# Optimization experiments

Hardware: AMD Instinct MI355X
Metric: run time of the kernel (lower is better)

## Reference

```python
import jax, jax.numpy as jnp
import numpy as np

# norse LIFParameters defaults with v_th overridden to 0.23
DT = 1e-3
TAU_SYN_INV = 200.0   # 1/5e-3
TAU_MEM_INV = 100.0   # 1/1e-2
V_TH = 0.23
ENC_V_TH = 1.0        # encoder uses default LIFParameters (v_th=1.0)
SEQ_LEN = 24
HIDDEN = 256
N_CLASSES = 10


def heaviside(x):
    return (x > 0).astype(x.dtype)


def encode(x):
    """ConstantCurrentLIFEncoder: lif_current_encoder over SEQ_LEN steps. x: [B, F] -> [T, B, F] spikes."""
    def step(v, _):
        v = v + DT * TAU_MEM_INV * (x - v)          # dv = dt*tau_mem_inv*((v_leak - v) + I)
        z = heaviside(v - ENC_V_TH)
        v = (1.0 - z) * v                            # reset to v_reset = 0
        return v, z
    _, zs = jax.lax.scan(step, jnp.zeros_like(x), None, length=SEQ_LEN)
    return zs


def lif_ff_step(inp, v, i):
    """norse lif_feed_forward_step: decay v with old i, decay i, spike, reset, then add input to i."""
    v_dec = v + DT * TAU_MEM_INV * (i - v)           # v_leak = 0
    i_dec = i * (1.0 - DT * TAU_SYN_INV)
    z = heaviside(v_dec - V_TH)
    v_new = (1.0 - z) * v_dec                        # v_reset = 0
    i_new = i_dec + inp
    return z, v_new, i_new


def setup_inputs() -> dict:
    key = jax.random.key(0)
    ks = jax.random.split(key, 8)
    B, F = 4096, 1024
    def lin(k, fan_in, fan_out):
        bound = 1.0 / np.sqrt(fan_in)
        kw, kb = jax.random.split(k)
        W = jax.random.uniform(kw, (fan_out, fan_in), jnp.float32, -bound, bound)
        b = jax.random.uniform(kb, (fan_out,), jnp.float32, -bound, bound)
        return W, b
    x = jax.random.normal(ks[0], (B, F), jnp.float32)
    W1, b1 = lin(ks[1], F, HIDDEN)
    W2, b2 = lin(ks[2], HIDDEN, HIDDEN)
    W3, b3 = lin(ks[3], HIDDEN, HIDDEN)
    Wli = jax.random.normal(ks[4], (N_CLASSES, HIDDEN), jnp.float32) * np.sqrt(2.0 / HIDDEN)
    return {"x": x, "W1": W1, "b1": b1, "W2": W2, "b2": b2, "W3": W3, "b3": b3, "Wli": Wli}


def reference(x, W1, b1, W2, b2, W3, b3, Wli):
    # dropout layers are identity in eval mode
    enc = encode(x)                                   # [T, B, F]
    B = x.shape[0]
    z2 = lambda d: jnp.zeros((B, d), x.dtype)
    carry0 = (z2(HIDDEN), z2(HIDDEN), z2(HIDDEN), z2(HIDDEN), z2(HIDDEN), z2(HIDDEN),
              z2(N_CLASSES), z2(N_CLASSES))
    def step(c, z):
        v1, i1, v2, i2, v3, i3, vo, io = c
        o1, v1, i1 = lif_ff_step(z @ W1.T + b1, v1, i1)
        o2, v2, i2 = lif_ff_step(o1 @ W2.T + b2, v2, i2)
        o2 = o2 + o1                                  # residual
        o3, v3, i3 = lif_ff_step(o2 @ W3.T + b3, v3, i3)
        o3 = o3 + o2                                  # residual
        # LILinearCell li_step: v from old i, i decays then accumulates W @ input (no bias)
        vo = vo + DT * TAU_MEM_INV * (io - vo)
        io = io * (1.0 - DT * TAU_SYN_INV) + o3 @ Wli.T
        return (v1, i1, v2, i2, v3, i3, vo, io), vo
    _, voltages = jax.lax.scan(step, carry0, enc)     # [T, B, n_classes]
    return voltages[-1]                               # decode = last timestep
```

## Files before the change

kernel.cpp:

```cpp
#include <hip/hip_runtime.h>
#include <hip/hip_bf16.h>

#define FEAT   1024
#define HID    256
#define TSTEPS 24
#define NCLS   10

typedef unsigned int u32;
typedef unsigned long long u64;
typedef unsigned short u16;

constexpr int OFF_W1T  = 0;
constexpr int OFF_W2T  = OFF_W1T + FEAT*HID;
constexpr int OFF_W3T  = OFF_W2T + HID*HID;
constexpr int OFF_WLI  = OFF_W3T + HID*HID;
constexpr int OFF_B1   = OFF_WLI + NCLS*HID;
constexpr int OFF_B2   = OFF_B1 + HID;
constexpr int OFF_B3   = OFF_B2 + HID;

struct CoefT { float c[TSTEPS]; };
constexpr CoefT make_coef() {
    CoefT r{};
    double c = 0.0, p9 = 1.0;
    r.c[TSTEPS-1] = 0.0f;
    for (int u = TSTEPS-1; u > 0; u--) {
        c = 0.8 * c + 0.1 * p9;
        p9 *= 0.9;
        r.c[u-1] = (float)c;
    }
    return r;
}
__device__ constexpr CoefT COEF = make_coef();

__device__ __forceinline__ u32 detect_bf16(const void* __restrict__ x, u32 lane) {
    float v = __bfloat162float(((const __hip_bfloat16*)x)[lane]);
    u64 bad = __ballot(!(fabsf(v) < 100.0f));
    return bad == 0ull ? 1u : 0u;
}

__device__ __forceinline__ float rd_any(const void* p, int idx, u32 isbf) {
    return isbf ? __bfloat162float(((const __hip_bfloat16*)p)[idx])
                : ((const float*)p)[idx];
}

__global__ __launch_bounds__(256) void prep_weights_k(const void* __restrict__ x,
        const void* W1, const void* W2, const void* W3, const void* Wli,
        const void* b1, const void* b2, const void* b3, float* __restrict__ ws) {
    const u32 isbf = detect_bf16(x, threadIdx.x & 63);
    const int b = blockIdx.x;
    const u32 tid = threadIdx.x;

    if (b == 96) {
        for (u32 e = tid; e < NCLS*HID; e += 256) ws[OFF_WLI + e] = rd_any(Wli, e, isbf);
        for (u32 e = tid; e < 3*HID; e += 256) {
            u32 which = e >> 8, idx = e & 255;
            const void* src = which == 0 ? b1 : (which == 1 ? b2 : b3);
            int off = which == 0 ? OFF_B1 : (which == 1 ? OFF_B2 : OFF_B3);
            ws[off + idx] = rd_any(src, idx, isbf);
        }
        return;
    }

    const void* src; float* dst; int srcW, h0, f0;
    if (b < 64)      { src = W1; dst = ws + OFF_W1T; srcW = FEAT; h0 = (b >> 4) * 64; f0 = (b & 15) * 64; }
    else if (b < 80) { int tb = b - 64; src = W2; dst = ws + OFF_W2T; srcW = HID; h0 = (tb >> 2) * 64; f0 = (tb & 3) * 64; }
    else             { int tb = b - 80; src = W3; dst = ws + OFF_W3T; srcW = HID; h0 = (tb >> 2) * 64; f0 = (tb & 3) * 64; }

    __shared__ float sm[64][65];
    const u32 c = tid & 63, r0 = tid >> 6;
    #pragma unroll
    for (int i = 0; i < 16; i++) {
        u32 r = r0 + 4 * i;
        sm[r][c] = rd_any(src, (h0 + r) * srcW + f0 + c, isbf);
    }
    __syncthreads();
    #pragma unroll
    for (int i = 0; i < 16; i++) {
        u32 r = r0 + 4 * i;
        dst[(size_t)(f0 + r) * HID + h0 + c] = sm[c][r];
    }
}

template<int SH, int MJ>
__device__ __forceinline__ void gather_stream(float acc[4], const float* __restrict__ Wt,
                                              u32 lm, u32 lane4) {
    u64 act = __ballot(lm != 0u);
    if (!act) return;
    u32 p = (u32)__builtin_ctzll(act); act &= act - 1;
    u32 cur = (u32)__builtin_amdgcn_readlane((int)lm, (int)p);
    for (;;) {
        u32 j = (u32)__builtin_ctz(cur); cur &= cur - 1;
        const u32 c0 = (p << SH) + (j & (u32)MJ);
        u32 c1 = c0, c2 = c0, c3 = c0;
        float f1 = 0.f, f2 = 0.f, f3 = 0.f;
        if (cur || act) {
            if (!cur) { p = (u32)__builtin_ctzll(act); act &= act - 1;
                        cur = (u32)__builtin_amdgcn_readlane((int)lm, (int)p); }
            j = (u32)__builtin_ctz(cur); cur &= cur - 1;
            c1 = (p << SH) + (j & (u32)MJ); f1 = 1.f;
        }
        if (cur || act) {
            if (!cur) { p = (u32)__builtin_ctzll(act); act &= act - 1;
                        cur = (u32)__builtin_amdgcn_readlane((int)lm, (int)p); }
            j = (u32)__builtin_ctz(cur); cur &= cur - 1;
            c2 = (p << SH) + (j & (u32)MJ); f2 = 1.f;
        }
        if (cur || act) {
            if (!cur) { p = (u32)__builtin_ctzll(act); act &= act - 1;
                        cur = (u32)__builtin_amdgcn_readlane((int)lm, (int)p); }
            j = (u32)__builtin_ctz(cur); cur &= cur - 1;
            c3 = (p << SH) + (j & (u32)MJ); f3 = 1.f;
        }
        const float4 w0 = *(const float4*)(Wt + ((size_t)c0 << 8) + lane4);
        const float4 w1 = *(const float4*)(Wt + ((size_t)c1 << 8) + lane4);
        const float4 w2 = *(const float4*)(Wt + ((size_t)c2 << 8) + lane4);
        const float4 w3 = *(const float4*)(Wt + ((size_t)c3 << 8) + lane4);
        acc[0] += w0.x; acc[1] += w0.y; acc[2] += w0.z; acc[3] += w0.w;
        acc[0] = fmaf(f1, w1.x, acc[0]); acc[1] = fmaf(f1, w1.y, acc[1]);
        acc[2] = fmaf(f1, w1.z, acc[2]); acc[3] = fmaf(f1, w1.w, acc[3]);
        acc[0] = fmaf(f2, w2.x, acc[0]); acc[1] = fmaf(f2, w2.y, acc[1]);
        acc[2] = fmaf(f2, w2.z, acc[2]); acc[3] = fmaf(f2, w2.w, acc[3]);
        acc[0] = fmaf(f3, w3.x, acc[0]); acc[1] = fmaf(f3, w3.y, acc[1]);
        acc[2] = fmaf(f3, w3.z, acc[2]); acc[3] = fmaf(f3, w3.w, acc[3]);
        if (!cur && !act) return;
        if (!cur) { p = (u32)__builtin_ctzll(act); act &= act - 1;
                    cur = (u32)__builtin_amdgcn_readlane((int)lm, (int)p); }
    }
}

__global__ __launch_bounds__(256) void snn_k(const void* __restrict__ xin,
                                             const float* __restrict__ ws,
                                             void* __restrict__ out) {
    const u32 tid  = threadIdx.x;
    const u32 lane = tid & 63;
    const u32 wv   = tid >> 6;
    const int row  = blockIdx.x * 4 + wv;
    const u32 lane4 = lane * 4;
    const u32 isbf = detect_bf16(xin, lane);

    const float* __restrict__ W1T = ws + OFF_W1T;
    const float* __restrict__ W2T = ws + OFF_W2T;
    const float* __restrict__ W3T = ws + OFF_W3T;
    const float* __restrict__ WLI = ws + OFF_WLI;

    __shared__ u32 sched[12 * 256];

    {
        float xv[16];
        if (isbf) {
            const uint4* xp = (const uint4*)((const u16*)xin + (size_t)row*FEAT + lane*16);
            uint4 A = xp[0], B = xp[1];
            u32 w[8] = {A.x, A.y, A.z, A.w, B.x, B.y, B.z, B.w};
            #pragma unroll
            for (int i = 0; i < 8; i++) {
                xv[2*i]   = __uint_as_float(w[i] << 16);
                xv[2*i+1] = __uint_as_float(w[i] & 0xffff0000u);
            }
        } else {
            const float4* xp = (const float4*)((const float*)xin + (size_t)row*FEAT + lane*16);
            float4 A = xp[0], B = xp[1], C = xp[2], D = xp[3];
            float tmp[16] = {A.x,A.y,A.z,A.w,B.x,B.y,B.z,B.w,C.x,C.y,C.z,C.w,D.x,D.y,D.z,D.w};
            #pragma unroll
            for (int i = 0; i < 16; i++) xv[i] = tmp[i];
        }
        u32 smreg[12];
        #pragma unroll
        for (int i = 0; i < 12; i++) smreg[i] = 0;
        #pragma unroll
        for (int j = 0; j < 16; j++) {
            float v = 0.f;
            #pragma unroll
            for (int t = 0; t < TSTEPS; t++) {
                v = v + 0.1f * (xv[j] - v);
                bool z = v > 1.0f;
                v = z ? 0.0f : v;
                if (z) smreg[t >> 1] |= 1u << (((t & 1) << 4) + j);
            }
        }
        #pragma unroll
        for (int i = 0; i < 12; i++) sched[i * 256 + tid] = smreg[i];
    }

    float v1[4], i1[4], v2[4], i2[4], v3[4], i3[4], g[4];
    #pragma unroll
    for (int k = 0; k < 4; k++) {
        v1[k]=0.f; i1[k]=0.f; v2[k]=0.f; i2[k]=0.f; v3[k]=0.f; i3[k]=0.f; g[k]=0.f;
    }
    const float4 b1v = *(const float4*)(ws + OFF_B1 + lane4);
    const float4 b2v = *(const float4*)(ws + OFF_B2 + lane4);
    const float4 b3v = *(const float4*)(ws + OFF_B3 + lane4);

    u32 pairreg = 0;
    for (int t = 0; t < TSTEPS; t++) {
        if ((t & 1) == 0) pairreg = sched[(t >> 1) * 256 + tid];
        const u32 lmE = (t & 1) ? (pairreg >> 16) : (pairreg & 0xffffu);

        float a1[4] = {b1v.x, b1v.y, b1v.z, b1v.w};
        gather_stream<4, 15>(a1, W1T, lmE, lane4);

        float o1v[4]; u32 lm1 = 0;
        #pragma unroll
        for (int kk = 0; kk < 4; kk++) {
            float vd = v1[kk] + 0.1f * (i1[kk] - v1[kk]);
            i1[kk] = i1[kk] * 0.8f;
            bool z = vd > 0.23f;
            v1[kk] = z ? 0.0f : vd;
            i1[kk] = i1[kk] + a1[kk];
            o1v[kk] = z ? 1.0f : 0.0f;
            lm1 |= (z ? 1u : 0u) << kk;
        }

        float a2[4] = {b2v.x, b2v.y, b2v.z, b2v.w};
        gather_stream<2, 3>(a2, W2T, lm1, lane4);

        float o2v[4]; u32 lm2 = 0;
        #pragma unroll
        for (int kk = 0; kk < 4; kk++) {
            float vd = v2[kk] + 0.1f * (i2[kk] - v2[kk]);
            i2[kk] = i2[kk] * 0.8f;
            bool z = vd > 0.23f;
            v2[kk] = z ? 0.0f : vd;
            i2[kk] = i2[kk] + a2[kk];
            o2v[kk] = (z ? 1.0f : 0.0f) + o1v[kk];
            lm2 |= (z ? 1u : 0u) << kk;
        }

        float a3[4] = {b3v.x, b3v.y, b3v.z, b3v.w};
        gather_stream<2, 3>(a3, W3T, lm2 | (lm1 << 4), lane4);

        const float cf = COEF.c[t];
        #pragma unroll
        for (int kk = 0; kk < 4; kk++) {
            float vd = v3[kk] + 0.1f * (i3[kk] - v3[kk]);
            i3[kk] = i3[kk] * 0.8f;
            bool z = vd > 0.23f;
            v3[kk] = z ? 0.0f : vd;
            i3[kk] = i3[kk] + a3[kk];
            float o3 = (z ? 1.0f : 0.0f) + o2v[kk];
            g[kk] += cf * o3;
        }
    }

    float s[NCLS];
    #pragma unroll
    for (int c = 0; c < NCLS; c++) {
        const float4 w = *(const float4*)(WLI + c*HID + lane4);
        float p = g[0]*w.x + g[1]*w.y + g[2]*w.z + g[3]*w.w;
        #pragma unroll
        for (int d = 32; d > 0; d >>= 1) p += __shfl_xor(p, d, 64);
        s[c] = p;
    }
    if (lane == 0) {
        if (isbf) {
            __hip_bfloat16* o = (__hip_bfloat16*)out + (size_t)row*NCLS;
            #pragma unroll
            for (int c = 0; c < NCLS; c++) o[c] = __float2bfloat16(s[c]);
        } else {
            float* o = (float*)out + (size_t)row*NCLS;
            #pragma unroll
            for (int c = 0; c < NCLS; c++) o[c] = s[c];
        }
    }
}

extern "C" void kernel_launch(void* const* d_in, const int* in_sizes, int n_in,
                              void* d_out, int out_size, void* d_ws, size_t ws_size,
                              hipStream_t stream) {
    const void* x   = d_in[0];
    const void* W1  = d_in[1];
    const void* b1  = d_in[2];
    const void* W2  = d_in[3];
    const void* b2  = d_in[4];
    const void* W3  = d_in[5];
    const void* b3  = d_in[6];
    const void* Wli = d_in[7];
    float* ws = (float*)d_ws;
    const int batch = in_sizes[0] / FEAT;

    prep_weights_k<<<97, 256, 0, stream>>>(x, W1, W2, W3, Wli, b1, b2, b3, ws);
    snn_k<<<batch/4, 256, 0, stream>>>(x, ws, d_out);
}
```

Before: 177.8 us.

## Build compacted spike index lists in LDS and gather weights in chunks of eight

Replaces the serial ballot/readlane spike iteration with a per-wave prefix-sum (mbcnt over popcount bits) that writes compacted active-column indices into shared memory, then gathers weight rows eight at a time with packed float2 accumulation. Layer 3 merges duplicate columns from the residual (o1+o2) into one entry with a multiplicity weight instead of two loads. The prep kernel also switches from an LDS-tiled transpose to a simple scattered-write transpose with more blocks. It adds LDS traffic and extra ballots per step but aims to remove scalar loop overhead and raise memory-level parallelism in the gathers.

```diff
diff --git a/kernel.cpp b/kernel.cpp
--- a/kernel.cpp
+++ b/kernel.cpp
@@ -9,6 +9,7 @@
 typedef unsigned int u32;
 typedef unsigned long long u64;
 typedef unsigned short u16;
+typedef float v2f __attribute__((ext_vector_type(2)));
 
 constexpr int OFF_W1T  = 0;
 constexpr int OFF_W2T  = OFF_W1T + FEAT*HID;
@@ -43,88 +44,129 @@
                 : ((const float*)p)[idx];
 }
 
-__global__ __launch_bounds__(256) void prep_weights_k(const void* __restrict__ x,
+__device__ __forceinline__ float4 rd4(const void* p, int i, u32 isbf) {
+    if (isbf) {
+        const u32* q = (const u32*)p;
+        u32 a = q[i >> 1], b = q[(i >> 1) + 1];
+        float4 r;
+        r.x = __uint_as_float(a << 16); r.y = __uint_as_float(a & 0xffff0000u);
+        r.z = __uint_as_float(b << 16); r.w = __uint_as_float(b & 0xffff0000u);
+        return r;
+    }
+    return ((const float4*)p)[i >> 2];
+}
+
+__global__ __launch_bounds__(256) void prep_k(const void* __restrict__ x,
         const void* W1, const void* W2, const void* W3, const void* Wli,
         const void* b1, const void* b2, const void* b3, float* __restrict__ ws) {
     const u32 isbf = detect_bf16(x, threadIdx.x & 63);
-    const int b = blockIdx.x;
-    const u32 tid = threadIdx.x;
-
-    if (b == 96) {
-        for (u32 e = tid; e < NCLS*HID; e += 256) ws[OFF_WLI + e] = rd_any(Wli, e, isbf);
-        for (u32 e = tid; e < 3*HID; e += 256) {
-            u32 which = e >> 8, idx = e & 255;
-            const void* src = which == 0 ? b1 : (which == 1 ? b2 : b3);
-            int off = which == 0 ? OFF_B1 : (which == 1 ? OFF_B2 : OFF_B3);
-            ws[off + idx] = rd_any(src, idx, isbf);
-        }
+    int b = blockIdx.x;
+    const u32 t = threadIdx.x;
+    if (b < 256) {
+        int id = b * 256 + t;
+        int h = id >> 8, f4 = (id & 255) << 2;
+        float4 w = rd4(W1, h * FEAT + f4, isbf);
+        float* d = ws + OFF_W1T;
+        d[(f4+0)*HID + h] = w.x; d[(f4+1)*HID + h] = w.y;
+        d[(f4+2)*HID + h] = w.z; d[(f4+3)*HID + h] = w.w;
         return;
     }
-
-    const void* src; float* dst; int srcW, h0, f0;
-    if (b < 64)      { src = W1; dst = ws + OFF_W1T; srcW = FEAT; h0 = (b >> 4) * 64; f0 = (b & 15) * 64; }
-    else if (b < 80) { int tb = b - 64; src = W2; dst = ws + OFF_W2T; srcW = HID; h0 = (tb >> 2) * 64; f0 = (tb & 3) * 64; }
-    else             { int tb = b - 80; src = W3; dst = ws + OFF_W3T; srcW = HID; h0 = (tb >> 2) * 64; f0 = (tb & 3) * 64; }
-
-    __shared__ float sm[64][65];
-    const u32 c = tid & 63, r0 = tid >> 6;
+    b -= 256;
+    if (b < 64) {
+        int id = b * 256 + t;
+        int h = id >> 6, f4 = (id & 63) << 2;
+        float4 w = rd4(W2, h * HID + f4, isbf);
+        float* d = ws + OFF_W2T;
+        d[(f4+0)*HID + h] = w.x; d[(f4+1)*HID + h] = w.y;
+        d[(f4+2)*HID + h] = w.z; d[(f4+3)*HID + h] = w.w;
+        return;
+    }
+    b -= 64;
+    if (b < 64) {
+        int id = b * 256 + t;
+        int h = id >> 6, f4 = (id & 63) << 2;
+        float4 w = rd4(W3, h * HID + f4, isbf);
+        float* d = ws + OFF_W3T;
+        d[(f4+0)*HID + h] = w.x; d[(f4+1)*HID + h] = w.y;
+        d[(f4+2)*HID + h] = w.z; d[(f4+3)*HID + h] = w.w;
+        return;
+    }
+    for (u32 e = t; e < NCLS*HID; e += 256) ws[OFF_WLI + e] = rd_any(Wli, e, isbf);
+    ws[OFF_B1 + t] = rd_any(b1, t, isbf);
+    ws[OFF_B2 + t] = rd_any(b2, t, isbf);
+    ws[OFF_B3 + t] = rd_any(b3, t, isbf);
+}
+
+__device__ __forceinline__ u32 mbcnt64(u64 m) {
+    return __builtin_amdgcn_mbcnt_hi((u32)(m >> 32),
+           __builtin_amdgcn_mbcnt_lo((u32)m, 0u));
+}
+
+
+__device__ __forceinline__ u32 build_list4(u16* list, u32 lmA, u32 lmB, u32 lane) {
+    u32 u = lmA | lmB;
+    u32 cnt = (u32)__builtin_popcount(u);
+    u64 B0 = __ballot((cnt & 1u) != 0);
+    u64 B1 = __ballot((cnt & 2u) != 0);
+    u64 B2 = __ballot((cnt & 4u) != 0);
+    u32 pos = mbcnt64(B0) + 2u*mbcnt64(B1) + 4u*mbcnt64(B2);
+    u32 n = (u32)__builtin_popcountll(B0) + 2u*(u32)__builtin_popcountll(B1)
+          + 4u*(u32)__builtin_popcountll(B2);
+    while (u) {
+        u32 j = (u32)__builtin_ctz(u); u &= u - 1;
+        u32 mult = ((lmA >> j) & 1u) + ((lmB >> j) & 1u);
+        list[pos++] = (u16)(((lane << 2) + j) | (mult << 12));
+    }
+    u32 pad = (8u - (n & 7u)) & 7u;
+    if (lane < pad) list[n + lane] = 0;
+    return n;
+}
+
+__device__ __forceinline__ u32 build_listE(u16* list, u32 lm, u32 lane) {
+    u32 cnt = (u32)__builtin_popcount(lm);
+    u32 pos = 0, n = 0;
     #pragma unroll
-    for (int i = 0; i < 16; i++) {
-        u32 r = r0 + 4 * i;
-        sm[r][c] = rd_any(src, (h0 + r) * srcW + f0 + c, isbf);
-    }
-    __syncthreads();
-    #pragma unroll
-    for (int i = 0; i < 16; i++) {
-        u32 r = r0 + 4 * i;
-        dst[(size_t)(f0 + r) * HID + h0 + c] = sm[c][r];
-    }
-}
-
-template<int SH, int MJ>
-__device__ __forceinline__ void gather_stream(float acc[4], const float* __restrict__ Wt,
-                                              u32 lm, u32 lane4) {
-    u64 act = __ballot(lm != 0u);
-    if (!act) return;
-    u32 p = (u32)__builtin_ctzll(act); act &= act - 1;
-    u32 cur = (u32)__builtin_amdgcn_readlane((int)lm, (int)p);
-    for (;;) {
-        u32 j = (u32)__builtin_ctz(cur); cur &= cur - 1;
-        const u32 c0 = (p << SH) + (j & (u32)MJ);
-        u32 c1 = c0, c2 = c0, c3 = c0;
-        float f1 = 0.f, f2 = 0.f, f3 = 0.f;
-        if (cur || act) {
-            if (!cur) { p = (u32)__builtin_ctzll(act); act &= act - 1;
-                        cur = (u32)__builtin_amdgcn_readlane((int)lm, (int)p); }
-            j = (u32)__builtin_ctz(cur); cur &= cur - 1;
-            c1 = (p << SH) + (j & (u32)MJ); f1 = 1.f;
-        }
-        if (cur || act) {
-            if (!cur) { p = (u32)__builtin_ctzll(act); act &= act - 1;
-                        cur = (u32)__builtin_amdgcn_readlane((int)lm, (int)p); }
-            j = (u32)__builtin_ctz(cur); cur &= cur - 1;
-            c2 = (p << SH) + (j & (u32)MJ); f2 = 1.f;
-        }
-        if (cur || act) {
-            if (!cur) { p = (u32)__builtin_ctzll(act); act &= act - 1;
-                        cur = (u32)__builtin_amdgcn_readlane((int)lm, (int)p); }
-            j = (u32)__builtin_ctz(cur); cur &= cur - 1;
-            c3 = (p << SH) + (j & (u32)MJ); f3 = 1.f;
-        }
-        const float4 w0 = *(const float4*)(Wt + ((size_t)c0 << 8) + lane4);
-        const float4 w1 = *(const float4*)(Wt + ((size_t)c1 << 8) + lane4);
-        const float4 w2 = *(const float4*)(Wt + ((size_t)c2 << 8) + lane4);
-        const float4 w3 = *(const float4*)(Wt + ((size_t)c3 << 8) + lane4);
-        acc[0] += w0.x; acc[1] += w0.y; acc[2] += w0.z; acc[3] += w0.w;
-        acc[0] = fmaf(f1, w1.x, acc[0]); acc[1] = fmaf(f1, w1.y, acc[1]);
-        acc[2] = fmaf(f1, w1.z, acc[2]); acc[3] = fmaf(f1, w1.w, acc[3]);
-        acc[0] = fmaf(f2, w2.x, acc[0]); acc[1] = fmaf(f2, w2.y, acc[1]);
-        acc[2] = fmaf(f2, w2.z, acc[2]); acc[3] = fmaf(f2, w2.w, acc[3]);
-        acc[0] = fmaf(f3, w3.x, acc[0]); acc[1] = fmaf(f3, w3.y, acc[1]);
-        acc[2] = fmaf(f3, w3.z, acc[2]); acc[3] = fmaf(f3, w3.w, acc[3]);
-        if (!cur && !act) return;
-        if (!cur) { p = (u32)__builtin_ctzll(act); act &= act - 1;
-                    cur = (u32)__builtin_amdgcn_readlane((int)lm, (int)p); }
+    for (int b = 0; b < 5; b++) {
+        u64 B = __ballot(((cnt >> b) & 1u) != 0);
+        pos += mbcnt64(B) << b;
+        n += ((u32)__builtin_popcountll(B)) << b;
+    }
+    while (lm) {
+        u32 j = (u32)__builtin_ctz(lm); lm &= lm - 1;
+        list[pos++] = (u16)(((lane << 4) + j) | 0x1000u);
+    }
+    u32 pad = (8u - (n & 7u)) & 7u;
+    if (lane < pad) list[n + lane] = 0;
+    return n;
+}
+
+#define GSTEP(E, W) do { \
+    float mm = (float)((E) >> 12); \
+    v2f mv = {mm, mm}; \
+    v2f lo = {(W).x, (W).y}, hi = {(W).z, (W).w}; \
+    accA += mv * lo; accB += mv * hi; \
+} while (0)
+
+__device__ __forceinline__ void gather_list(v2f& accA, v2f& accB,
+        const float* __restrict__ Wt, const u16* list, u32 n, u32 lane4) {
+    u32 nch = (n + 7u) >> 3;
+    const uint4* lp = (const uint4*)list;
+    for (u32 c = 0; c < nch; c++) {
+        uint4 d = lp[c];
+        u32 e0 = d.x & 0xffffu, e1 = d.x >> 16;
+        u32 e2 = d.y & 0xffffu, e3 = d.y >> 16;
+        u32 e4 = d.z & 0xffffu, e5 = d.z >> 16;
+        u32 e6 = d.w & 0xffffu, e7 = d.w >> 16;
+        const float4 w0 = *(const float4*)(Wt + ((e0 & 0xfffu) << 8) + lane4);
+        const float4 w1 = *(const float4*)(Wt + ((e1 & 0xfffu) << 8) + lane4);
+        const float4 w2 = *(const float4*)(Wt + ((e2 & 0xfffu) << 8) + lane4);
+        const float4 w3 = *(const float4*)(Wt + ((e3 & 0xfffu) << 8) + lane4);
+        const float4 w4 = *(const float4*)(Wt + ((e4 & 0xfffu) << 8) + lane4);
+        const float4 w5 = *(const float4*)(Wt + ((e5 & 0xfffu) << 8) + lane4);
+        const float4 w6 = *(const float4*)(Wt + ((e6 & 0xfffu) << 8) + lane4);
+        const float4 w7 = *(const float4*)(Wt + ((e7 & 0xfffu) << 8) + lane4);
+        GSTEP(e0, w0); GSTEP(e1, w1); GSTEP(e2, w2); GSTEP(e3, w3);
+        GSTEP(e4, w4); GSTEP(e5, w5); GSTEP(e6, w6); GSTEP(e7, w7);
     }
 }
 
@@ -144,6 +186,8 @@
     const float* __restrict__ WLI = ws + OFF_WLI;
 
     __shared__ u32 sched[12 * 256];
+    __shared__ __align__(16) u16 listE[4][1040];
+    __shared__ __align__(16) u16 listL[4][272];
 
     {
         float xv[16];
@@ -190,13 +234,18 @@
     const float4 b2v = *(const float4*)(ws + OFF_B2 + lane4);
     const float4 b3v = *(const float4*)(ws + OFF_B3 + lane4);
 
+    u16* const lE = listE[wv];
+    u16* const lL = listL[wv];
+
     u32 pairreg = 0;
     for (int t = 0; t < TSTEPS; t++) {
         if ((t & 1) == 0) pairreg = sched[(t >> 1) * 256 + tid];
         const u32 lmE = (t & 1) ? (pairreg >> 16) : (pairreg & 0xffffu);
 
-        float a1[4] = {b1v.x, b1v.y, b1v.z, b1v.w};
-        gather_stream<4, 15>(a1, W1T, lmE, lane4);
+        u32 nE = build_listE(lE, lmE, lane);
+        v2f accA = {b1v.x, b1v.y}, accB = {b1v.z, b1v.w};
+        gather_list(accA, accB, W1T, lE, nE, lane4);
+        float a1[4] = {accA.x, accA.y, accB.x, accB.y};
 
         float o1v[4]; u32 lm1 = 0;
         #pragma unroll
@@ -210,8 +259,10 @@
             lm1 |= (z ? 1u : 0u) << kk;
         }
 
-        float a2[4] = {b2v.x, b2v.y, b2v.z, b2v.w};
-        gather_stream<2, 3>(a2, W2T, lm1, lane4);
+        u32 n1 = build_list4(lL, lm1, 0u, lane);
+        accA = (v2f){b2v.x, b2v.y}; accB = (v2f){b2v.z, b2v.w};
+        gather_list(accA, accB, W2T, lL, n1, lane4);
+        float a2[4] = {accA.x, accA.y, accB.x, accB.y};
 
         float o2v[4]; u32 lm2 = 0;
         #pragma unroll
@@ -225,8 +276,10 @@
             lm2 |= (z ? 1u : 0u) << kk;
         }
 
-        float a3[4] = {b3v.x, b3v.y, b3v.z, b3v.w};
-        gather_stream<2, 3>(a3, W3T, lm2 | (lm1 << 4), lane4);
+        u32 n2 = build_list4(lL, lm1, lm2, lane);
+        accA = (v2f){b3v.x, b3v.y}; accB = (v2f){b3v.z, b3v.w};
+        gather_list(accA, accB, W3T, lL, n2, lane4);
+        float a3[4] = {accA.x, accA.y, accB.x, accB.y};
 
         const float cf = COEF.c[t];
         #pragma unroll
@@ -277,6 +330,6 @@
     float* ws = (float*)d_ws;
     const int batch = in_sizes[0] / FEAT;
 
-    prep_weights_k<<<97, 256, 0, stream>>>(x, W1, W2, W3, Wli, b1, b2, b3, ws);
+    prep_k<<<385, 256, 0, stream>>>(x, W1, W2, W3, Wli, b1, b2, b3, ws);
     snn_k<<<batch/4, 256, 0, stream>>>(x, ws, d_out);
 }
```

After: 156.8 us. 1.13x faster.
